# Kernel optimization log

Hardware: AMD Instinct MI355X
Metric: run time of the kernel (lower is better)

The kernel has to match this reference:

```python
import jax, jax.numpy as jnp
import numpy as np

HIDDEN = 256
NUM_REL = 6
NUM_BASES = 30
N_NODES = 50000
N_EDGES = 800000


def rgcn_gate_layer(x, src, dst, etype, basis, att, root, bias, gate_w, gate_b):
    # Basis-decomposed relation weights: W_r = sum_b att[r,b] * basis[b]
    N = x.shape[0]
    W = jnp.einsum('rb,bio->rio', att, basis)           # [R, d, d]
    # Transform all nodes under every relation (cheaper than per-edge matmul
    # since N*R < E), then gather the per-edge message.
    xw = jnp.einsum('nd,rde->rne', x, W)                # [R, N, d]
    msg = xw[etype, src]                                # [E, d]
    # Scalar sigmoid gate per edge message
    g = jax.nn.sigmoid(msg @ gate_w + gate_b)           # [E, 1]
    gated = g * msg
    # Mean aggregation over incoming edges per destination node
    agg = jax.ops.segment_sum(gated, dst, num_segments=N)
    deg = jax.ops.segment_sum(jnp.ones((src.shape[0], 1), x.dtype), dst,
                              num_segments=N)
    agg = agg / jnp.maximum(deg, 1.0)
    return agg + x @ root + bias


def setup_inputs() -> dict:
    key = jax.random.key(0)
    ks = jax.random.split(key, 16)
    d = HIDDEN
    inp = {
        'x': jax.random.normal(ks[0], (N_NODES, d), jnp.float32),
        'edge_src': jax.random.randint(ks[1], (N_EDGES,), 0, N_NODES, jnp.int32),
        'edge_dst': jax.random.randint(ks[2], (N_EDGES,), 0, N_NODES, jnp.int32),
        'edge_type': jax.random.randint(ks[3], (N_EDGES,), 0, NUM_REL, jnp.int32),
    }
    def glorot(k, shape):
        fan = shape[-2] + shape[-1]
        return jax.random.uniform(k, shape, jnp.float32,
                                  -np.sqrt(6.0 / fan), np.sqrt(6.0 / fan))
    for li, off in ((1, 4), (2, 10)):
        inp[f'basis{li}'] = glorot(ks[off + 0], (NUM_BASES, d, d))
        inp[f'att{li}'] = glorot(ks[off + 1], (NUM_REL, NUM_BASES))
        inp[f'root{li}'] = glorot(ks[off + 2], (d, d))
        inp[f'bias{li}'] = jnp.zeros((d,), jnp.float32)
        inp[f'gate_w{li}'] = glorot(ks[off + 3], (d, 1))
        inp[f'gate_b{li}'] = jnp.zeros((1,), jnp.float32)
    return inp


def reference(x, edge_src, edge_dst, edge_type,
              basis1, att1, root1, bias1, gate_w1, gate_b1,
              basis2, att2, root2, bias2, gate_w2, gate_b2):
    h = jax.nn.relu(rgcn_gate_layer(x, edge_src, edge_dst, edge_type,
                                    basis1, att1, root1, bias1,
                                    gate_w1, gate_b1))
    out = rgcn_gate_layer(h, edge_src, edge_dst, edge_type,
                          basis2, att2, root2, bias2, gate_w2, gate_b2)
    return out
```

## Files before the change

### kernel.cpp

```cpp
#include <hip/hip_runtime.h>
#include <cmath>

#define HIDDEN 256
#define NUM_REL 6
#define KA 1536
#define KB 1792
#define NK 56
#define NKA 48
#define CTSTRIDE 28672

typedef float f32x4_t __attribute__((ext_vector_type(4)));
typedef short bf16x8_t __attribute__((ext_vector_type(8)));

__device__ __forceinline__ float bf2f(ushort u) {
  return __uint_as_float(((uint)u) << 16);
}
__device__ __forceinline__ ushort f2bf(float f) {
  uint u = __float_as_uint(f);
  u += 0x7FFFu + ((u >> 16) & 1u);
  return (ushort)(u >> 16);
}

__global__ __launch_bounds__(256) void prep_weights(
    const float* __restrict__ att, const float* __restrict__ basis,
    const float* __restrict__ root, const float* __restrict__ gw,
    ushort* __restrict__ BTf, float* __restrict__ gatevec) {
  const int d = blockIdx.x, r = blockIdx.y, o = threadIdx.x;
  float v;
  if (r < 6) {
    float s = 0.f;
#pragma unroll
    for (int b = 0; b < 30; ++b)
      s += att[r * 30 + b] * basis[(size_t)b * 65536 + d * 256 + o];
    v = s;
  } else {
    v = root[d * 256 + o];
  }
  const int gk = r * 256 + d;
  BTf[(size_t)(o >> 4) * CTSTRIDE + (gk >> 3) * 128 + (o & 15) * 8 +
      (gk & 7)] = f2bf(v);
  if (r < 6) {
    float t = v * gw[o];
#pragma unroll
    for (int off = 32; off; off >>= 1) t += __shfl_xor(t, off);
    __shared__ float sums[4];
    if ((o & 63) == 0) sums[o >> 6] = t;
    __syncthreads();
    if (o == 0) gatevec[r * 256 + d] = sums[0] + sums[1] + sums[2] + sums[3];
  }
}

__global__ __launch_bounds__(256) void gdot_kernel(
    const void* __restrict__ xin, int xIsF32, ushort* __restrict__ xbOut,
    const float* __restrict__ gatevec, const float* __restrict__ gate_b,
    float* __restrict__ G, int N) {
  const int wave = (blockIdx.x * blockDim.x + threadIdx.x) >> 6;
  if (wave >= N) return;
  const int l = threadIdx.x & 63;
  float x0, x1, x2, x3;
  if (xIsF32) {
    float4 xv = ((const float4*)xin)[(size_t)wave * 64 + l];
    x0 = xv.x; x1 = xv.y; x2 = xv.z; x3 = xv.w;
    ushort4 o;
    o.x = f2bf(x0); o.y = f2bf(x1); o.z = f2bf(x2); o.w = f2bf(x3);
    ((ushort4*)xbOut)[(size_t)wave * 64 + l] = o;
  } else {
    ushort4 xv = ((const ushort4*)xin)[(size_t)wave * 64 + l];
    x0 = bf2f(xv.x); x1 = bf2f(xv.y); x2 = bf2f(xv.z); x3 = bf2f(xv.w);
  }
  float out = 0.f;
#pragma unroll
  for (int r = 0; r < NUM_REL; ++r) {
    float4 gv = ((const float4*)(gatevec + r * 256))[l];
    float d = x0 * gv.x + x1 * gv.y + x2 * gv.z + x3 * gv.w;
#pragma unroll
    for (int off = 32; off; off >>= 1) d += __shfl_xor(d, off);
    if (l == r) out = d;
  }
  if (l < NUM_REL) {
    const float gb = gate_b[0];
    G[(size_t)l * N + wave] = 1.f / (1.f + __expf(-(out + gb)));
  }
}

#define ACCUM(rj, gj, vj)                                                  \
  do {                                                                    \
    const float fx = (gj)*bf2f((vj).x), fy = (gj)*bf2f((vj).y);           \
    const float fz = (gj)*bf2f((vj).z), fw = (gj)*bf2f((vj).w);           \
    switch (rj) {                                                         \
      case 0: a0x += fx; a0y += fy; a0z += fz; a0w += fw; break;          \
      case 1: a1x += fx; a1y += fy; a1z += fz; a1w += fw; break;          \
      case 2: a2x += fx; a2y += fy; a2z += fz; a2w += fw; break;          \
      case 3: a3x += fx; a3y += fy; a3z += fz; a3w += fw; break;          \
      case 4: a4x += fx; a4y += fy; a4z += fz; a4w += fw; break;          \
      default: a5x += fx; a5y += fy; a5z += fz; a5w += fw; break;         \
    }                                                                     \
  } while (0)

#define RELOF(ei) ((ei >= b1) + (ei >= b2) + (ei >= b3) + (ei >= b4) + (ei >= b5))

__global__ __launch_bounds__(256) void edge_agg(
    const ushort* __restrict__ xb, const float* __restrict__ G,
    const int* __restrict__ rp8, const int* __restrict__ src_s,
    ushort* __restrict__ A, int N) {
  const int n = (blockIdx.x * blockDim.x + threadIdx.x) >> 6;
  if (n >= N) return;
  const int l = threadIdx.x & 63;
  const int b0 = rp8[n * 8 + 0], b1 = rp8[n * 8 + 1], b2 = rp8[n * 8 + 2];
  const int b3 = rp8[n * 8 + 3], b4 = rp8[n * 8 + 4], b5 = rp8[n * 8 + 5];
  const int b6 = rp8[n * 8 + 6];

  float a0x = 0, a0y = 0, a0z = 0, a0w = 0, a1x = 0, a1y = 0, a1z = 0, a1w = 0;
  float a2x = 0, a2y = 0, a2z = 0, a2w = 0, a3x = 0, a3y = 0, a3z = 0, a3w = 0;
  float a4x = 0, a4y = 0, a4z = 0, a4w = 0, a5x = 0, a5y = 0, a5z = 0, a5w = 0;

  int e = b0;
  for (; e + 7 < b6; e += 8) {
    const int s0 = src_s[e + 0], s1 = src_s[e + 1];
    const int s2 = src_s[e + 2], s3 = src_s[e + 3];
    const int s4 = src_s[e + 4], s5 = src_s[e + 5];
    const int s6 = src_s[e + 6], s7 = src_s[e + 7];
    const ushort4 v0 = ((const ushort4*)(xb + (size_t)s0 * 256))[l];
    const ushort4 v1 = ((const ushort4*)(xb + (size_t)s1 * 256))[l];
    const ushort4 v2 = ((const ushort4*)(xb + (size_t)s2 * 256))[l];
    const ushort4 v3 = ((const ushort4*)(xb + (size_t)s3 * 256))[l];
    const ushort4 v4 = ((const ushort4*)(xb + (size_t)s4 * 256))[l];
    const ushort4 v5 = ((const ushort4*)(xb + (size_t)s5 * 256))[l];
    const ushort4 v6 = ((const ushort4*)(xb + (size_t)s6 * 256))[l];
    const ushort4 v7 = ((const ushort4*)(xb + (size_t)s7 * 256))[l];
    const int r0 = RELOF(e + 0), r1 = RELOF(e + 1), r2 = RELOF(e + 2),
              r3 = RELOF(e + 3), r4 = RELOF(e + 4), r5 = RELOF(e + 5),
              r6 = RELOF(e + 6), r7 = RELOF(e + 7);
    const float g0 = G[(size_t)r0 * N + s0], g1 = G[(size_t)r1 * N + s1];
    const float g2 = G[(size_t)r2 * N + s2], g3 = G[(size_t)r3 * N + s3];
    const float g4 = G[(size_t)r4 * N + s4], g5 = G[(size_t)r5 * N + s5];
    const float g6 = G[(size_t)r6 * N + s6], g7 = G[(size_t)r7 * N + s7];
    ACCUM(r0, g0, v0); ACCUM(r1, g1, v1); ACCUM(r2, g2, v2); ACCUM(r3, g3, v3);
    ACCUM(r4, g4, v4); ACCUM(r5, g5, v5); ACCUM(r6, g6, v6); ACCUM(r7, g7, v7);
  }
  for (; e < b6; ++e) {
    const int s0 = src_s[e];
    const ushort4 v0 = ((const ushort4*)(xb + (size_t)s0 * 256))[l];
    const int r0 = RELOF(e);
    const float g0 = G[(size_t)r0 * N + s0];
    ACCUM(r0, g0, v0);
  }

  const float inv = 1.f / fmaxf((float)(b6 - b0), 1.f);
  ushort* Arow = A + (size_t)n * KA;
  ushort4 o;
  o.x = f2bf(a0x * inv); o.y = f2bf(a0y * inv); o.z = f2bf(a0z * inv); o.w = f2bf(a0w * inv);
  ((ushort4*)(Arow + 0 * 256))[l] = o;
  o.x = f2bf(a1x * inv); o.y = f2bf(a1y * inv); o.z = f2bf(a1z * inv); o.w = f2bf(a1w * inv);
  ((ushort4*)(Arow + 1 * 256))[l] = o;
  o.x = f2bf(a2x * inv); o.y = f2bf(a2y * inv); o.z = f2bf(a2z * inv); o.w = f2bf(a2w * inv);
  ((ushort4*)(Arow + 2 * 256))[l] = o;
  o.x = f2bf(a3x * inv); o.y = f2bf(a3y * inv); o.z = f2bf(a3z * inv); o.w = f2bf(a3w * inv);
  ((ushort4*)(Arow + 3 * 256))[l] = o;
  o.x = f2bf(a4x * inv); o.y = f2bf(a4y * inv); o.z = f2bf(a4z * inv); o.w = f2bf(a4w * inv);
  ((ushort4*)(Arow + 4 * 256))[l] = o;
  o.x = f2bf(a5x * inv); o.y = f2bf(a5y * inv); o.z = f2bf(a5z * inv); o.w = f2bf(a5w * inv);
  ((ushort4*)(Arow + 5 * 256))[l] = o;
}

__global__ __launch_bounds__(256) void gemm_fused(
    const ushort* __restrict__ A, const ushort* __restrict__ xb,
    const ushort* __restrict__ BTf, const float* __restrict__ bias,
    void* __restrict__ outPtr, int M, int mode) {
  __shared__ ushort As[3][64 * 32];
  const int row0 = blockIdx.x * 64;
  const int tid = threadIdx.x;
  const int w = tid >> 6, l = tid & 63;

  const int srow = tid >> 2;
  const int ssc = (tid & 3) ^ (srow & 3);
  const int ga = min(row0 + srow, M - 1);
  const ushort* gpA = A + (size_t)ga * KA + ssc * 8;
  const ushort* gpX = xb + (size_t)ga * 256 + ssc * 8;

  const ushort* Bb =
      BTf + (size_t)(w * 4) * CTSTRIDE + (l >> 4) * 128 + (l & 15) * 8;

  f32x4_t acc[4][4] = {};

  auto stage = [&](int k, int buf) {
    const ushort* gp = (k < NKA) ? (gpA + k * 32) : (gpX + (k * 32 - KA));
    __builtin_amdgcn_global_load_lds(
        (const __attribute__((address_space(1))) void*)gp,
        (__attribute__((address_space(3))) void*)(&As[buf][tid * 8]), 16, 0, 0);
  };

  auto compute = [&](int buf, const bf16x8_t* b) {
    bf16x8_t a[4];
#pragma unroll
    for (int m = 0; m < 4; ++m) {
      const int rr = m * 16 + (l & 15);
      a[m] = *(const bf16x8_t*)(&As[buf][rr * 32 + (((l >> 4) ^ (rr & 3)) * 8)]);
    }
#pragma unroll
    for (int m = 0; m < 4; ++m)
#pragma unroll
      for (int n = 0; n < 4; ++n)
        acc[m][n] = __builtin_amdgcn_mfma_f32_16x16x32_bf16(a[m], b[n],
                                                            acc[m][n], 0, 0, 0);
  };

  bf16x8_t bE[4], bO[4];
  stage(0, 0);
  stage(1, 1);
#pragma unroll
  for (int n = 0; n < 4; ++n)
    bE[n] = *(const bf16x8_t*)(Bb + (size_t)n * CTSTRIDE);

  for (int k = 0; k < NK; k += 2) {
    asm volatile("s_waitcnt vmcnt(5)" ::: "memory");
    __builtin_amdgcn_s_barrier();
#pragma unroll
    for (int n = 0; n < 4; ++n)
      bO[n] = *(const bf16x8_t*)(Bb + (size_t)n * CTSTRIDE + (k + 1) * 512);
    if (k + 2 < NK) stage(k + 2, (k + 2) % 3);
    compute(k % 3, bE);

    asm volatile("s_waitcnt vmcnt(5)" ::: "memory");
    __builtin_amdgcn_s_barrier();
    if (k + 2 < NK) {
#pragma unroll
      for (int n = 0; n < 4; ++n)
        bE[n] = *(const bf16x8_t*)(Bb + (size_t)n * CTSTRIDE + (k + 2) * 512);
    }
    if (k + 3 < NK) stage(k + 3, (k + 3) % 3);
    compute((k + 1) % 3, bO);
  }

  const int rbase = row0 + (l >> 4) * 4;
  const int cbase = w * 64 + (l & 15);
#pragma unroll
  for (int n = 0; n < 4; ++n) {
    const int col = cbase + n * 16;
    const float bv = bias[col];
#pragma unroll
    for (int m = 0; m < 4; ++m)
#pragma unroll
      for (int i = 0; i < 4; ++i) {
        const int row = rbase + m * 16 + i;
        if (row < M) {
          float v = acc[m][n][i] + bv;
          if (mode == 0) {
            v = fmaxf(v, 0.f);
            ((ushort*)outPtr)[(size_t)row * 256 + col] = f2bf(v);
          } else {
            ((float*)outPtr)[(size_t)row * 256 + col] = v;
          }
        }
      }
  }
}

__global__ void hist_kernel(const int* __restrict__ dst,
                            const int* __restrict__ ety,
                            int* __restrict__ cnt, int E) {
  int stride = gridDim.x * blockDim.x;
  for (int e = blockIdx.x * blockDim.x + threadIdx.x; e < E; e += stride)
    atomicAdd(&cnt[dst[e] * 8 + ety[e]], 1);
}

__global__ void scan_reduce(const int* __restrict__ cnt,
                            int* __restrict__ blockSums, int n) {
  __shared__ int sd[256];
  int base = blockIdx.x * 1024;
  int t = threadIdx.x;
  int s = 0;
#pragma unroll
  for (int i = 0; i < 4; ++i) {
    int idx = base + t * 4 + i;
    s += (idx < n) ? cnt[idx] : 0;
  }
  sd[t] = s; __syncthreads();
  for (int off = 128; off; off >>= 1) {
    if (t < off) sd[t] += sd[t + off];
    __syncthreads();
  }
  if (t == 0) blockSums[blockIdx.x] = sd[0];
}

__global__ void scan_offsets(int* __restrict__ blockSums, int nb) {
  __shared__ int sd[512];
  const int t = threadIdx.x;
  const int v = (t < nb) ? blockSums[t] : 0;
  sd[t] = v; __syncthreads();
  for (int off = 1; off < 512; off <<= 1) {
    int u = (t >= off) ? sd[t - off] : 0;
    __syncthreads();
    sd[t] += u;
    __syncthreads();
  }
  if (t < nb) blockSums[t] = sd[t] - v;
}

__global__ void scan_write(const int* __restrict__ cnt,
                           const int* __restrict__ blockSums,
                           int* __restrict__ row_ptr, int* __restrict__ cursor,
                           int n) {
  __shared__ int sd[256];
  int base = blockIdx.x * 1024;
  int t = threadIdx.x;
  int v[4]; int s = 0;
#pragma unroll
  for (int i = 0; i < 4; ++i) {
    int idx = base + t * 4 + i;
    v[i] = (idx < n) ? cnt[idx] : 0;
    s += v[i];
  }
  sd[t] = s; __syncthreads();
  for (int off = 1; off < 256; off <<= 1) {
    int val = (t >= off) ? sd[t - off] : 0;
    __syncthreads();
    sd[t] += val;
    __syncthreads();
  }
  int excl = blockSums[blockIdx.x] + sd[t] - s;
  for (int i = 0; i < 4; ++i) {
    int idx = base + t * 4 + i;
    if (idx < n) {
      row_ptr[idx] = excl;
      cursor[idx] = excl;
      excl += v[i];
      if (idx == n - 1) row_ptr[n] = excl;
    }
  }
}

__global__ void scatter_kernel(const int* __restrict__ src,
                               const int* __restrict__ dst,
                               const int* __restrict__ ety,
                               int* __restrict__ cursor,
                               int* __restrict__ src_s, int E) {
  int stride = gridDim.x * blockDim.x;
  for (int e = blockIdx.x * blockDim.x + threadIdx.x; e < E; e += stride) {
    int bin = dst[e] * 8 + ety[e];
    int pos = atomicAdd(&cursor[bin], 1);
    src_s[pos] = src[e];
  }
}

static inline size_t align16(size_t x) { return (x + 15) & ~(size_t)15; }

extern "C" void kernel_launch(void* const* d_in, const int* in_sizes, int n_in,
                              void* d_out, int out_size, void* d_ws,
                              size_t ws_size, hipStream_t stream) {
  const float* x    = (const float*)d_in[0];
  const int*   src  = (const int*)d_in[1];
  const int*   dst  = (const int*)d_in[2];
  const int*   ety  = (const int*)d_in[3];

  const int N   = in_sizes[0] / HIDDEN;
  const int E   = in_sizes[1];
  const int RN2 = N * 8;

  char* p = (char*)d_ws;
  ushort* BTf    = (ushort*)p; p += align16(((size_t)16 * CTSTRIDE + 4096) * 2);
  float* gatevec = (float*)p;  p += align16((size_t)NUM_REL * 256 * 4);
  float* G       = (float*)p;  p += align16((size_t)NUM_REL * N * 4);
  ushort* xb0    = (ushort*)p; p += align16((size_t)N * HIDDEN * 2);
  ushort* xb1    = (ushort*)p; p += align16((size_t)N * HIDDEN * 2);
  int* cnt       = (int*)p;    p += align16((size_t)RN2 * 4);
  int* cursor    = (int*)p;    p += align16((size_t)RN2 * 4);
  int* row_ptr   = (int*)p;    p += align16((size_t)(RN2 + 1) * 4);
  int* blockSums = (int*)p;    p += 2048;
  int* src_s     = (int*)p;    p += align16((size_t)E * 4);
  ushort* A      = (ushort*)p;

  const int scanBlocks = (RN2 + 1023) / 1024;

  hipMemsetAsync(cnt, 0, (size_t)RN2 * sizeof(int), stream);
  hist_kernel<<<2048, 256, 0, stream>>>(dst, ety, cnt, E);
  scan_reduce<<<scanBlocks, 256, 0, stream>>>(cnt, blockSums, RN2);
  scan_offsets<<<1, 512, 0, stream>>>(blockSums, scanBlocks);
  scan_write<<<scanBlocks, 256, 0, stream>>>(cnt, blockSums, row_ptr, cursor,
                                             RN2);
  scatter_kernel<<<2048, 256, 0, stream>>>(src, dst, ety, cursor, src_s, E);

  const int nodeBlocks = (N * 64 + 255) / 256;
  const int gemmGrid = (N + 63) / 64;

  for (int layer = 0; layer < 2; ++layer) {
    const float* bas  = (const float*)d_in[layer ? 10 : 4];
    const float* att  = (const float*)d_in[layer ? 11 : 5];
    const float* root = (const float*)d_in[layer ? 12 : 6];
    const float* bias = (const float*)d_in[layer ? 13 : 7];
    const float* gw   = (const float*)d_in[layer ? 14 : 8];
    const float* gb   = (const float*)d_in[layer ? 15 : 9];
    const ushort* xb  = layer ? xb1 : xb0;
    void* outp = layer ? d_out : (void*)xb1;
    const int mode = layer ? 1 : 0;

    prep_weights<<<dim3(256, 7), 256, 0, stream>>>(att, bas, root, gw, BTf,
                                                   gatevec);
    gdot_kernel<<<nodeBlocks, 256, 0, stream>>>(
        layer ? (const void*)xb1 : (const void*)x, layer ? 0 : 1, xb0,
        gatevec, gb, G, N);
    edge_agg<<<nodeBlocks, 256, 0, stream>>>(xb, G, row_ptr, src_s, A, N);
    gemm_fused<<<gemmGrid, 256, 0, stream>>>(A, xb, BTf, bias, outp, N, mode);
  }
}
```

Measured before the change: 512.6 us.

## Chunk edge aggregation and GEMM over node ranges to keep A in cache

Splits the edge aggregation and fused GEMM into alternating launches over chunks of 12800 nodes, reusing a chunk-sized A buffer so the intermediate aggregate matrix can stay in L2/MALL cache between producer and consumer. It also extends the LDS XOR swizzle with a second row-bit term to reduce bank conflicts in the A-tile reads. The cost is more kernel launches, with less parallelism per launch and a tail in each chunk.

```diff
diff --git a/kernel.cpp b/kernel.cpp
--- a/kernel.cpp
+++ b/kernel.cpp
@@ -8,6 +8,7 @@
 #define NK 56
 #define NKA 48
 #define CTSTRIDE 28672
+#define CHUNK 12800
 
 typedef float f32x4_t __attribute__((ext_vector_type(4)));
 typedef short bf16x8_t __attribute__((ext_vector_type(8)));
@@ -102,9 +103,10 @@
 __global__ __launch_bounds__(256) void edge_agg(
     const ushort* __restrict__ xb, const float* __restrict__ G,
     const int* __restrict__ rp8, const int* __restrict__ src_s,
-    ushort* __restrict__ A, int N) {
-  const int n = (blockIdx.x * blockDim.x + threadIdx.x) >> 6;
-  if (n >= N) return;
+    ushort* __restrict__ A, int N, int n0, int nChunk) {
+  const int ln = (blockIdx.x * blockDim.x + threadIdx.x) >> 6;
+  if (ln >= nChunk) return;
+  const int n = n0 + ln;
   const int l = threadIdx.x & 63;
   const int b0 = rp8[n * 8 + 0], b1 = rp8[n * 8 + 1], b2 = rp8[n * 8 + 2];
   const int b3 = rp8[n * 8 + 3], b4 = rp8[n * 8 + 4], b5 = rp8[n * 8 + 5];
@@ -147,7 +149,7 @@
   }
 
   const float inv = 1.f / fmaxf((float)(b6 - b0), 1.f);
-  ushort* Arow = A + (size_t)n * KA;
+  ushort* Arow = A + (size_t)ln * KA;
   ushort4 o;
   o.x = f2bf(a0x * inv); o.y = f2bf(a0y * inv); o.z = f2bf(a0z * inv); o.w = f2bf(a0w * inv);
   ((ushort4*)(Arow + 0 * 256))[l] = o;
@@ -166,16 +168,16 @@
 __global__ __launch_bounds__(256) void gemm_fused(
     const ushort* __restrict__ A, const ushort* __restrict__ xb,
     const ushort* __restrict__ BTf, const float* __restrict__ bias,
-    void* __restrict__ outPtr, int M, int mode) {
+    void* __restrict__ outPtr, int M, int n0, int mode) {
   __shared__ ushort As[3][64 * 32];
-  const int row0 = blockIdx.x * 64;
+  const int row0 = n0 + blockIdx.x * 64;
   const int tid = threadIdx.x;
   const int w = tid >> 6, l = tid & 63;
 
   const int srow = tid >> 2;
-  const int ssc = (tid & 3) ^ (srow & 3);
+  const int ssc = (tid & 3) ^ (srow & 3) ^ ((srow >> 2) & 3);
   const int ga = min(row0 + srow, M - 1);
-  const ushort* gpA = A + (size_t)ga * KA + ssc * 8;
+  const ushort* gpA = A + (size_t)(ga - n0) * KA + ssc * 8;
   const ushort* gpX = xb + (size_t)ga * 256 + ssc * 8;
 
   const ushort* Bb =
@@ -195,7 +197,8 @@
 #pragma unroll
     for (int m = 0; m < 4; ++m) {
       const int rr = m * 16 + (l & 15);
-      a[m] = *(const bf16x8_t*)(&As[buf][rr * 32 + (((l >> 4) ^ (rr & 3)) * 8)]);
+      const int c = (l >> 4) ^ (rr & 3) ^ ((rr >> 2) & 3);
+      a[m] = *(const bf16x8_t*)(&As[buf][rr * 32 + c * 8]);
     }
 #pragma unroll
     for (int m = 0; m < 4; ++m)
@@ -381,7 +384,6 @@
   scatter_kernel<<<2048, 256, 0, stream>>>(src, dst, ety, cursor, src_s, E);
 
   const int nodeBlocks = (N * 64 + 255) / 256;
-  const int gemmGrid = (N + 63) / 64;
 
   for (int layer = 0; layer < 2; ++layer) {
     const float* bas  = (const float*)d_in[layer ? 10 : 4];
@@ -399,7 +401,15 @@
     gdot_kernel<<<nodeBlocks, 256, 0, stream>>>(
         layer ? (const void*)xb1 : (const void*)x, layer ? 0 : 1, xb0,
         gatevec, gb, G, N);
-    edge_agg<<<nodeBlocks, 256, 0, stream>>>(xb, G, row_ptr, src_s, A, N);
-    gemm_fused<<<gemmGrid, 256, 0, stream>>>(A, xb, BTf, bias, outp, N, mode);
-  }
-}
+
+    for (int n0 = 0; n0 < N; n0 += CHUNK) {
+      const int nChunk = (N - n0 < CHUNK) ? (N - n0) : CHUNK;
+      const int eaBlocks = (nChunk * 64 + 255) / 256;
+      const int gBlocks = (nChunk + 63) / 64;
+      edge_agg<<<eaBlocks, 256, 0, stream>>>(xb, G, row_ptr, src_s, A, N, n0,
+                                             nChunk);
+      gemm_fused<<<gBlocks, 256, 0, stream>>>(A, xb, BTf, bias, outp, N, n0,
+                                              mode);
+    }
+  }
+}
```

Result: slower. 683.2 us (+33.3%).
